# Kernel optimization log

Measured on AMD Instinct MI355X. Metric: run time of the kernel, lower is better.

## Reference

```python
import jax, jax.numpy as jnp
import numpy as np

OUT = 7          # roi_align output_size
NUM_ANCHORS = 27 # 3 scales x 3 ratios x 3 angles
MAX_PROPOSALS = 100
RPN_STRIDE = 32


def conv2d(x, w, b, stride=1, pad=1):
    y = jax.lax.conv_general_dilated(
        x, w, (stride, stride), [(pad, pad), (pad, pad)],
        dimension_numbers=('NCHW', 'OIHW', 'NCHW'))
    return y + b[None, :, None, None]


def generate_anchors(H, W, stride):
    # matches CustomOrientedRPN.generate_anchors
    sx = np.arange(0, W * stride, stride, dtype=np.float32)
    sy = np.arange(0, H * stride, stride, dtype=np.float32)
    SY, SX = np.meshgrid(sy, sx, indexing='ij')
    shifts = np.stack([SX, SY], axis=-1).reshape(-1, 2)  # [HW,2]
    base = []
    for scale in (32.0, 64.0, 128.0):
        for ratio in (0.5, 1.0, 2.0):
            w = scale * ratio ** 0.5
            h = scale / ratio ** 0.5
            for angle in (0.0, 45.0, 90.0):
                base.append([w, h, angle])
    base = np.array(base, dtype=np.float32)  # [A,3]
    A = base.shape[0]
    anchors = np.concatenate(
        [np.repeat(shifts[:, None, :], A, axis=1),
         np.broadcast_to(base[None], (shifts.shape[0], A, 3))], axis=-1)
    return jnp.asarray(anchors.reshape(-1, 5))  # [HW*A, 5]


def rotated_roi_align(features, boxes, batch_idx):
    # Vectorized version of the per-box affine_grid + grid_sample loop
    # (align_corners=False semantics for both, zero padding for grid_sample).
    B, C, Hf, Wf = features.shape
    lin = (2.0 * jnp.arange(OUT, dtype=features.dtype) + 1.0) / OUT - 1.0
    ys, xs = jnp.meshgrid(lin, lin, indexing='ij')  # [7,7] base grid

    cx, cy, w, h, ang = (boxes[:, i] for i in range(5))
    ar = -ang * jnp.pi / 180.0
    c, s = jnp.cos(ar), jnp.sin(ar)
    t00 = w / Wf * c; t01 = -h / Hf * s; t02 = 2.0 * cx / Wf - 1.0
    t10 = w / Wf * s; t11 = h / Hf * c;  t12 = 2.0 * cy / Hf - 1.0
    gx = t00[:, None, None] * xs + t01[:, None, None] * ys + t02[:, None, None]  # [N,7,7]
    gy = t10[:, None, None] * xs + t11[:, None, None] * ys + t12[:, None, None]

    ix = ((gx + 1.0) * Wf - 1.0) / 2.0
    iy = ((gy + 1.0) * Hf - 1.0) / 2.0
    x0 = jnp.floor(ix); y0 = jnp.floor(iy)
    wx = ix - x0;       wy = iy - y0
    x0i = x0.astype(jnp.int32); y0i = y0.astype(jnp.int32)

    def gather(dx, dy, wgt):
        xi = x0i + dx; yi = y0i + dy
        valid = (xi >= 0) & (xi < Wf) & (yi >= 0) & (yi < Hf)
        xc = jnp.clip(xi, 0, Wf - 1)
        yc = jnp.clip(yi, 0, Hf - 1)
        def one(bi, yb, xb):
            return features[bi][:, yb, xb]  # [C,7,7]
        vals = jax.vmap(one)(batch_idx, yc, xc)  # [N,C,7,7]
        return vals * (wgt * valid)[:, None, :, :]

    return (gather(0, 0, (1 - wx) * (1 - wy)) + gather(1, 0, wx * (1 - wy)) +
            gather(0, 1, (1 - wx) * wy) + gather(1, 1, wx * wy))


def setup_inputs() -> dict:
    key = jax.random.key(0)
    ks = jax.random.split(key, 20)

    def w(k, shape):
        fan_in = int(np.prod(shape[1:]))
        return jax.random.normal(k, shape, jnp.float32) / np.sqrt(fan_in)

    C = 256; A = NUM_ANCHORS; NC = 5
    return {
        'images': jax.random.normal(ks[0], (8, 3, 1024, 1024), jnp.float32),
        'backbone_w': w(ks[1], (C, 3, 3, 3)),   'backbone_b': jnp.zeros((C,), jnp.float32),
        'rpn_conv_w': w(ks[2], (256, C, 3, 3)), 'rpn_conv_b': jnp.zeros((256,), jnp.float32),
        'obj_w': w(ks[3], (A, 256, 1, 1)),      'obj_b': jnp.zeros((A,), jnp.float32),
        'delta_w': w(ks[4], (A * 5, 256, 1, 1)) * 0.1, 'delta_b': jnp.zeros((A * 5,), jnp.float32),
        'fc1_w': w(ks[5], (1024, C * OUT * OUT)), 'fc1_b': jnp.zeros((1024,), jnp.float32),
        'fc2_w': w(ks[6], (1024, 1024)),          'fc2_b': jnp.zeros((1024,), jnp.float32),
        'cls_w': w(ks[7], (NC, 1024)),            'cls_b': jnp.zeros((NC,), jnp.float32),
        'bbox_w': w(ks[8], (5, 1024)),            'bbox_b': jnp.zeros((5,), jnp.float32),
    }


def reference(images, backbone_w, backbone_b, rpn_conv_w, rpn_conv_b,
              obj_w, obj_b, delta_w, delta_b,
              fc1_w, fc1_b, fc2_w, fc2_b, cls_w, cls_b, bbox_w, bbox_b):
    # backbone (stand-in: single stride-16 conv)
    f = conv2d(images, backbone_w, backbone_b, stride=16, pad=1)  # [B,256,64,64]
    B, C, H, W = f.shape
    # F.interpolate(scale_factor=0.5, bilinear, align_corners=False) == 2x2 mean
    f = f.reshape(B, C, H // 2, 2, W // 2, 2).mean(axis=(3, 5))   # [B,256,32,32]
    Hf, Wf = f.shape[2], f.shape[3]

    # RPN
    t = jax.nn.relu(conv2d(f, rpn_conv_w, rpn_conv_b, 1, 1))
    _logits = conv2d(t, obj_w, obj_b, 1, 0)  # computed as in original (unused downstream)
    deltas = conv2d(t, delta_w, delta_b, 1, 0)  # [B, A*5, Hf, Wf]
    A = NUM_ANCHORS
    deltas = deltas.reshape(B, A, 5, Hf, Wf).transpose(0, 3, 4, 1, 2).reshape(B, -1, 5)

    anchors = generate_anchors(Hf, Wf, RPN_STRIDE)  # [HW*A,5]
    acx, acy, aw, ah, aa = (anchors[:, i] for i in range(5))
    pcx = deltas[:, :, 0] * aw + acx
    pcy = deltas[:, :, 1] * ah + acy
    pw = jnp.exp(deltas[:, :, 2]) * aw
    ph = jnp.exp(deltas[:, :, 3]) * ah
    pa = aa + deltas[:, :, 4]
    proposals = jnp.stack([pcx, pcy, pw, ph, pa], axis=-1)  # [B, HW*A, 5]
    proposals = proposals[:, :MAX_PROPOSALS]                # p[:max_proposals]

    boxes = proposals.reshape(-1, 5)                        # [B*100, 5]
    batch_idx = jnp.repeat(jnp.arange(B), MAX_PROPOSALS)
    pooled = rotated_roi_align(f, boxes, batch_idx)         # [B*100, 256, 7, 7]

    x = pooled.reshape(pooled.shape[0], -1)
    x = jax.nn.relu(x @ fc1_w.T + fc1_b)
    x = jax.nn.relu(x @ fc2_w.T + fc2_b)
    class_logits = x @ cls_w.T + cls_b
    obb_preds = x @ bbox_w.T + bbox_b
    return class_logits, obb_preds
```

## Files before the change

### kernel.cpp

```cpp
#include <hip/hip_runtime.h>
#include <hip/hip_bf16.h>

using bf16 = __hip_bfloat16;

typedef __attribute__((ext_vector_type(8))) short bf16x8;
typedef __attribute__((ext_vector_type(4))) float f32x4;

__device__ __forceinline__ void async16(const void* g, void* l) {
  __builtin_amdgcn_global_load_lds(
      (const __attribute__((address_space(1))) unsigned int*)g,
      (__attribute__((address_space(3))) unsigned int*)l, 16, 0, 0);
}

__device__ __forceinline__ void store_o(float* C, size_t i, float v) { C[i] = v; }
__device__ __forceinline__ void store_o(bf16* C, size_t i, float v) {
  C[i] = __float2bfloat16(v);
}

__global__ __launch_bounds__(256) void k_backbone(const float* __restrict__ img,
    const float* __restrict__ w, const float* __restrict__ bias,
    float* __restrict__ f) {
  int blk = blockIdx.x;
  int x = blk & 31, y = (blk >> 5) & 31, b = blk >> 10;
  __shared__ float patch[4 * 27];
  int t = threadIdx.x;
  if (t < 108) {
    int kx = t % 3, ky = (t / 3) % 3, cin = (t / 9) % 3, sub = t / 27;
    int sy = sub >> 1, sx = sub & 1;
    int iy = (2 * y + sy) * 16 - 1 + ky;
    int ix = (2 * x + sx) * 16 - 1 + kx;
    float v = 0.f;
    if (iy >= 0 && ix >= 0)
      v = img[((size_t)(b * 3 + cin) * 1024 + iy) * 1024 + ix];
    patch[t] = v;
  }
  __syncthreads();
  int c = t;
  float wr[27];
#pragma unroll
  for (int k = 0; k < 27; ++k) wr[k] = w[c * 27 + k];
  float acc = 0.f;
#pragma unroll
  for (int sub = 0; sub < 4; ++sub)
#pragma unroll
    for (int k = 0; k < 27; ++k)
      acc += patch[sub * 27 + k] * wr[k];
  f[(size_t)blk * 256 + c] = acc * 0.25f + bias[c];
}

__global__ __launch_bounds__(256) void k_rpn(const float* __restrict__ f,
    const float* __restrict__ rpn_w, float* __restrict__ part) {
  int p = blockIdx.x;
  int kc = blockIdx.y;
  int x = p & 3, b = p >> 2;
  __shared__ float fpl[6][16];
  int tid = threadIdx.x;
  if (tid < 96) {
    int cin2 = tid & 15;
    int rc = tid >> 4;
    int row = rc / 3, col = rc % 3;
    int xc = x - 1 + col;
    float v = 0.f;
    if (xc >= 0)
      v = f[((size_t)(b * 32 + row) * 32 + xc) * 256 + kc * 16 + cin2];
    fpl[rc][cin2] = v;
  }
  __syncthreads();
  int c = tid;
  const float* wbase = rpn_w + (size_t)c * 2304 + kc * 144;
  float acc = 0.f;
#pragma unroll
  for (int cin2 = 0; cin2 < 16; ++cin2) {
    const float* wp = wbase + cin2 * 9;
    acc += fpl[0][cin2] * wp[3] + fpl[1][cin2] * wp[4]
         + fpl[2][cin2] * wp[5] + fpl[3][cin2] * wp[6]
         + fpl[4][cin2] * wp[7] + fpl[5][cin2] * wp[8];
  }
  part[((size_t)kc * 32 + p) * 256 + c] = acc;
}

__global__ __launch_bounds__(512) void k_delta(const float* __restrict__ part,
    const float* __restrict__ rpn_b,
    const float* __restrict__ dw, const float* __restrict__ db,
    float* __restrict__ boxes) {
  int p = blockIdx.x;
  int x = p & 3, b = p >> 2;
  __shared__ float tbuf[256];
  __shared__ float dvals[135];
  int tid = threadIdx.x;
  if (tid < 256) {
    float s = rpn_b[tid];
#pragma unroll
    for (int kc = 0; kc < 16; ++kc)
      s += part[((size_t)kc * 32 + p) * 256 + tid];
    tbuf[tid] = fmaxf(s, 0.f);
  }
  __syncthreads();
  if (tid < 270) {
    int o = tid >> 1, half = tid & 1;
    const float* wp = dw + (size_t)o * 256 + half * 128;
    const float* tp = tbuf + half * 128;
    float s = 0.f;
#pragma unroll 8
    for (int k = 0; k < 128; ++k) s += tp[k] * wp[k];
    s += __shfl_xor(s, 1, 64);
    if (half == 0) dvals[o] = s + db[o];
  }
  __syncthreads();
  if (tid < 27) {
    int i = x * 27 + tid;
    if (i < 100) {
      int a = tid;
      int si = a / 9, ri = (a / 3) % 3, ai = a % 3;
      float scale = 32.f * (float)(1 << si);
      float sr = (ri == 0) ? 0.70710678118654752f : (ri == 1 ? 1.0f : 1.41421356237309505f);
      float aw = scale * sr, ah = scale / sr;
      float aang = 45.f * (float)ai;
      float acx = 32.f * (float)x, acy = 0.f;
      float* bx = boxes + (size_t)(b * 100 + i) * 5;
      bx[0] = dvals[a * 5 + 0] * aw + acx;
      bx[1] = dvals[a * 5 + 1] * ah + acy;
      bx[2] = expf(dvals[a * 5 + 2]) * aw;
      bx[3] = expf(dvals[a * 5 + 3]) * ah;
      bx[4] = aang + dvals[a * 5 + 4];
    }
  }
}

__global__ __launch_bounds__(256) void k_roialign(const float* __restrict__ f,
    const float* __restrict__ boxes, bf16* __restrict__ pooled) {
  int n = blockIdx.x;
  int b = n / 100;
  __shared__ int six[49], siy[49];
  __shared__ float swx[49], swy[49];
  __shared__ float pool_s[12544];
  int tid = threadIdx.x;
  if (tid < 49) {
    float cx = boxes[n * 5 + 0], cy = boxes[n * 5 + 1];
    float w = boxes[n * 5 + 2], h = boxes[n * 5 + 3], ang = boxes[n * 5 + 4];
    float ar = -ang * 0.017453292519943295f;
    float cc = cosf(ar), ss = sinf(ar);
    float t00 = w * (1.f / 32.f) * cc, t01 = -h * (1.f / 32.f) * ss;
    float t02 = cx * (2.f / 32.f) - 1.f;
    float t10 = w * (1.f / 32.f) * ss, t11 = h * (1.f / 32.f) * cc;
    float t12 = cy * (2.f / 32.f) - 1.f;
    int py = tid / 7, px = tid - py * 7;
    float lx = (2.f * px + 1.f) * (1.f / 7.f) - 1.f;
    float ly = (2.f * py + 1.f) * (1.f / 7.f) - 1.f;
    float gx = t00 * lx + t01 * ly + t02;
    float gy = t10 * lx + t11 * ly + t12;
    float ix = ((gx + 1.f) * 32.f - 1.f) * 0.5f;
    float iy = ((gy + 1.f) * 32.f - 1.f) * 0.5f;
    float x0 = floorf(ix), y0 = floorf(iy);
    six[tid] = (int)x0; siy[tid] = (int)y0;
    swx[tid] = ix - x0; swy[tid] = iy - y0;
  }
  __syncthreads();
  const float* fb = f + (size_t)b * 262144;
  int c = tid;
  for (int bin = 0; bin < 49; ++bin) {
    int x0 = six[bin], y0 = siy[bin];
    float wx = swx[bin], wy = swy[bin];
    float acc = 0.f;
    if (x0 >= 0 && x0 < 32 && y0 >= 0 && y0 < 32)
      acc += fb[(y0 * 32 + x0) * 256 + c] * ((1.f - wx) * (1.f - wy));
    if (x0 + 1 >= 0 && x0 + 1 < 32 && y0 >= 0 && y0 < 32)
      acc += fb[(y0 * 32 + x0 + 1) * 256 + c] * (wx * (1.f - wy));
    if (x0 >= 0 && x0 < 32 && y0 + 1 >= 0 && y0 + 1 < 32)
      acc += fb[((y0 + 1) * 32 + x0) * 256 + c] * ((1.f - wx) * wy);
    if (x0 + 1 >= 0 && x0 + 1 < 32 && y0 + 1 >= 0 && y0 + 1 < 32)
      acc += fb[((y0 + 1) * 32 + x0 + 1) * 256 + c] * (wx * wy);
    pool_s[c * 49 + bin] = acc;
  }
  __syncthreads();
  bf16* po = pooled + (size_t)n * 12544;
  for (int k = tid; k < 12544; k += 256) po[k] = __float2bfloat16(pool_s[k]);
}

__global__ __launch_bounds__(256) void k_gemm_sk(
    const unsigned short* __restrict__ A, const float* __restrict__ B,
    float* __restrict__ P, int M, int N, int K, int KC) {
  __shared__ unsigned short As[64 * 64];
  __shared__ unsigned short Bs[64 * 72];
  int t = threadIdx.x;
  int wv = t >> 6, ln = t & 63;
  int quad = ln >> 4, l15 = ln & 15;
  int n0 = blockIdx.x * 64, m0 = blockIdx.y * 64;
  int kbeg = blockIdx.z * KC;
  int kend = kbeg + KC; if (kend > K) kend = K;

  int arow = wv * 8 + (ln >> 3);
  int sg = (ln & 7) ^ (arow & 7);
  int r0 = m0 + arow;      if (r0 > M - 1) r0 = M - 1;
  int r1 = m0 + arow + 32; if (r1 > M - 1) r1 = M - 1;
  const unsigned short* Ap0 = A + (size_t)r0 * K + sg * 8;
  const unsigned short* Ap1 = A + (size_t)r1 * K + sg * 8;
  unsigned short* ldsA0 = &As[wv * 512];
  unsigned short* ldsA1 = &As[2048 + wv * 512];

  int brow = t >> 2, bq = t & 3;
  const float* Bp = B + (size_t)(n0 + brow) * K + bq * 16;
  unsigned short* bdst = &Bs[brow * 72 + bq * 16];

  f32x4 acc[4];
#pragma unroll
  for (int j = 0; j < 4; ++j) acc[j] = (f32x4){0.f, 0.f, 0.f, 0.f};

  int mrow = wv * 16 + l15;

  for (int k0 = kbeg; k0 < kend; k0 += 64) {
    float4 bv0 = *(const float4*)(Bp + k0);
    float4 bv1 = *(const float4*)(Bp + k0 + 4);
    float4 bv2 = *(const float4*)(Bp + k0 + 8);
    float4 bv3 = *(const float4*)(Bp + k0 + 12);
    __syncthreads();
    async16(Ap0 + k0, ldsA0);
    async16(Ap1 + k0, ldsA1);
    unsigned short bb[16];
    bb[0]  = __bfloat16_as_ushort(__float2bfloat16(bv0.x));
    bb[1]  = __bfloat16_as_ushort(__float2bfloat16(bv0.y));
    bb[2]  = __bfloat16_as_ushort(__float2bfloat16(bv0.z));
    bb[3]  = __bfloat16_as_ushort(__float2bfloat16(bv0.w));
    bb[4]  = __bfloat16_as_ushort(__float2bfloat16(bv1.x));
    bb[5]  = __bfloat16_as_ushort(__float2bfloat16(bv1.y));
    bb[6]  = __bfloat16_as_ushort(__float2bfloat16(bv1.z));
    bb[7]  = __bfloat16_as_ushort(__float2bfloat16(bv1.w));
    bb[8]  = __bfloat16_as_ushort(__float2bfloat16(bv2.x));
    bb[9]  = __bfloat16_as_ushort(__float2bfloat16(bv2.y));
    bb[10] = __bfloat16_as_ushort(__float2bfloat16(bv2.z));
    bb[11] = __bfloat16_as_ushort(__float2bfloat16(bv2.w));
    bb[12] = __bfloat16_as_ushort(__float2bfloat16(bv3.x));
    bb[13] = __bfloat16_as_ushort(__float2bfloat16(bv3.y));
    bb[14] = __bfloat16_as_ushort(__float2bfloat16(bv3.z));
    bb[15] = __bfloat16_as_ushort(__float2bfloat16(bv3.w));
#pragma unroll
    for (int u = 0; u < 2; ++u)
      *(bf16x8*)(bdst + u * 8) = *(const bf16x8*)(bb + u * 8);
    __syncthreads();
#pragma unroll
    for (int ks = 0; ks < 2; ++ks) {
      bf16x8 a = *(const bf16x8*)&As[mrow * 64 + (((ks * 4 + quad) ^ (mrow & 7)) * 8)];
#pragma unroll
      for (int j = 0; j < 4; ++j) {
        bf16x8 b = *(const bf16x8*)&Bs[(j * 16 + l15) * 72 + ks * 32 + quad * 8];
        acc[j] = __builtin_amdgcn_mfma_f32_16x16x32_bf16(a, b, acc[j], 0, 0, 0);
      }
    }
  }
  float* Pz = P + (size_t)blockIdx.z * M * N;
#pragma unroll
  for (int j = 0; j < 4; ++j) {
    int n = n0 + j * 16 + l15;
#pragma unroll
    for (int r = 0; r < 4; ++r) {
      int m = m0 + wv * 16 + quad * 4 + r;
      if (m < M) Pz[(size_t)m * N + n] = acc[j][r];
    }
  }
}

template <typename OutT, int KS>
__global__ __launch_bounds__(256) void k_reduce(const float* __restrict__ P,
    const float* __restrict__ bias, OutT* __restrict__ C, int MN, int N) {
  int i = blockIdx.x * 256 + threadIdx.x;
  if (i * 4 >= MN) return;
  f32x4 s = *(const f32x4*)(P + (size_t)i * 4);
#pragma unroll
  for (int z = 1; z < KS; ++z)
    s += *(const f32x4*)(P + (size_t)z * MN + i * 4);
  int n = (i * 4) % N;
#pragma unroll
  for (int u = 0; u < 4; ++u)
    store_o(C, (size_t)i * 4 + u, fmaxf(s[u] + bias[n + u], 0.f));
}

__global__ __launch_bounds__(640) void k_heads(const float* __restrict__ x2,
    const float* __restrict__ cls_w, const float* __restrict__ cls_b,
    const float* __restrict__ bbox_w, const float* __restrict__ bbox_b,
    float* __restrict__ out) {
  int n = blockIdx.x;
  int wave = threadIdx.x >> 6;
  int lane = threadIdx.x & 63;
  const float* w = (wave < 5) ? (cls_w + (size_t)wave * 1024)
                              : (bbox_w + (size_t)(wave - 5) * 1024);
  const float* xr = x2 + (size_t)n * 1024;
  float s = 0.f;
  for (int k = lane; k < 1024; k += 64) s += xr[k] * w[k];
  for (int off = 32; off; off >>= 1) s += __shfl_down(s, off, 64);
  if (lane == 0) {
    int o = (wave < 5) ? wave : wave - 5;
    float bias = (wave < 5) ? cls_b[o] : bbox_b[o];
    int base = (wave < 5) ? 0 : 4000;
    out[base + n * 5 + o] = s + bias;
  }
}

extern "C" void kernel_launch(void* const* d_in, const int* in_sizes, int n_in,
                              void* d_out, int out_size, void* d_ws, size_t ws_size,
                              hipStream_t stream) {
  const float* images     = (const float*)d_in[0];
  const float* backbone_w = (const float*)d_in[1];
  const float* backbone_b = (const float*)d_in[2];
  const float* rpn_w      = (const float*)d_in[3];
  const float* rpn_b      = (const float*)d_in[4];
  const float* delta_w    = (const float*)d_in[7];
  const float* delta_b    = (const float*)d_in[8];
  const float* fc1_w      = (const float*)d_in[9];
  const float* fc1_b      = (const float*)d_in[10];
  const float* fc2_w      = (const float*)d_in[11];
  const float* fc2_b      = (const float*)d_in[12];
  const float* cls_w      = (const float*)d_in[13];
  const float* cls_b      = (const float*)d_in[14];
  const float* bbox_w     = (const float*)d_in[15];
  const float* bbox_b     = (const float*)d_in[16];

  char* ws = (char*)d_ws;
  float* f      = (float*)ws;
  float* boxes  = (float*)(ws + 8388608);
  bf16*  pooled = (bf16*) (ws + 8404992);
  bf16*  x1     = (bf16*) (ws + 28475392);
  float* x2     = (float*)(ws + 30113792);
  float* parts  = (float*)(ws + 33390592);
  float* rpart = parts;

  k_backbone<<<8192, 256, 0, stream>>>(images, backbone_w, backbone_b, f);
  k_rpn<<<dim3(32, 16), 256, 0, stream>>>(f, rpn_w, rpart);
  k_delta<<<32, 512, 0, stream>>>(rpart, rpn_b, delta_w, delta_b, boxes);
  k_roialign<<<800, 256, 0, stream>>>(f, boxes, pooled);

  k_gemm_sk<<<dim3(16, 13, 6), 256, 0, stream>>>(
      (const unsigned short*)pooled, fc1_w, parts, 800, 1024, 12544, 2112);
  k_reduce<bf16, 6><<<800, 256, 0, stream>>>(parts, fc1_b, x1, 819200, 1024);

  k_gemm_sk<<<dim3(16, 13, 4), 256, 0, stream>>>(
      (const unsigned short*)x1, fc2_w, parts, 800, 1024, 1024, 256);
  k_reduce<float, 4><<<800, 256, 0, stream>>>(parts, fc2_b, x2, 819200, 1024);

  k_heads<<<800, 640, 0, stream>>>(x2, cls_w, cls_b, bbox_w, bbox_b, (float*)d_out);
}
```

Measured before the change: 353.9 us.

## Enlarge split-K GEMM M-tile to 128 with 2x2 warp layout

The split-K GEMM block tile grows from 64x64 to 128x64, and the four waves are arranged 2x2 so each computes a 64x32 sub-tile with 4x2 MFMA fragments. Each fp32 B (weight) tile, which is loaded and converted to bf16 per block, is now reused across twice as many rows. That halves the number of blocks along M (13 to 7) and the redundant weight reads and conversions. The cost is more accumulator registers, more LDS, fewer blocks in the grid, and more padded rows (896 vs 800).

```diff
diff --git a/kernel.cpp b/kernel.cpp
--- a/kernel.cpp
+++ b/kernel.cpp
@@ -180,33 +180,35 @@
 __global__ __launch_bounds__(256) void k_gemm_sk(
     const unsigned short* __restrict__ A, const float* __restrict__ B,
     float* __restrict__ P, int M, int N, int K, int KC) {
-  __shared__ unsigned short As[64 * 64];
+  __shared__ unsigned short As[128 * 64];
   __shared__ unsigned short Bs[64 * 72];
   int t = threadIdx.x;
   int wv = t >> 6, ln = t & 63;
   int quad = ln >> 4, l15 = ln & 15;
-  int n0 = blockIdx.x * 64, m0 = blockIdx.y * 64;
+  int wm = wv >> 1, wn = wv & 1;
+  int n0 = blockIdx.x * 64, m0 = blockIdx.y * 128;
   int kbeg = blockIdx.z * KC;
   int kend = kbeg + KC; if (kend > K) kend = K;
 
-  int arow = wv * 8 + (ln >> 3);
-  int sg = (ln & 7) ^ (arow & 7);
-  int r0 = m0 + arow;      if (r0 > M - 1) r0 = M - 1;
-  int r1 = m0 + arow + 32; if (r1 > M - 1) r1 = M - 1;
-  const unsigned short* Ap0 = A + (size_t)r0 * K + sg * 8;
-  const unsigned short* Ap1 = A + (size_t)r1 * K + sg * 8;
-  unsigned short* ldsA0 = &As[wv * 512];
-  unsigned short* ldsA1 = &As[2048 + wv * 512];
+  int srow = ln >> 3;
+  int sg = (ln & 7) ^ srow;
+  const unsigned short* Ap[4];
+#pragma unroll
+  for (int q = 0; q < 4; ++q) {
+    int r = m0 + q * 32 + wv * 8 + srow;
+    if (r > M - 1) r = M - 1;
+    Ap[q] = A + (size_t)r * K + sg * 8;
+  }
 
   int brow = t >> 2, bq = t & 3;
   const float* Bp = B + (size_t)(n0 + brow) * K + bq * 16;
   unsigned short* bdst = &Bs[brow * 72 + bq * 16];
 
-  f32x4 acc[4];
-#pragma unroll
-  for (int j = 0; j < 4; ++j) acc[j] = (f32x4){0.f, 0.f, 0.f, 0.f};
-
-  int mrow = wv * 16 + l15;
+  f32x4 acc[4][2];
+#pragma unroll
+  for (int mf = 0; mf < 4; ++mf)
+#pragma unroll
+    for (int nf = 0; nf < 2; ++nf) acc[mf][nf] = (f32x4){0.f, 0.f, 0.f, 0.f};
 
   for (int k0 = kbeg; k0 < kend; k0 += 64) {
     float4 bv0 = *(const float4*)(Bp + k0);
@@ -214,8 +216,9 @@
     float4 bv2 = *(const float4*)(Bp + k0 + 8);
     float4 bv3 = *(const float4*)(Bp + k0 + 12);
     __syncthreads();
-    async16(Ap0 + k0, ldsA0);
-    async16(Ap1 + k0, ldsA1);
+#pragma unroll
+    for (int q = 0; q < 4; ++q)
+      async16(Ap[q] + k0, &As[q * 2048 + wv * 512]);
     unsigned short bb[16];
     bb[0]  = __bfloat16_as_ushort(__float2bfloat16(bv0.x));
     bb[1]  = __bfloat16_as_ushort(__float2bfloat16(bv0.y));
@@ -239,22 +242,32 @@
     __syncthreads();
 #pragma unroll
     for (int ks = 0; ks < 2; ++ks) {
-      bf16x8 a = *(const bf16x8*)&As[mrow * 64 + (((ks * 4 + quad) ^ (mrow & 7)) * 8)];
-#pragma unroll
-      for (int j = 0; j < 4; ++j) {
-        bf16x8 b = *(const bf16x8*)&Bs[(j * 16 + l15) * 72 + ks * 32 + quad * 8];
-        acc[j] = __builtin_amdgcn_mfma_f32_16x16x32_bf16(a, b, acc[j], 0, 0, 0);
+      bf16x8 a[4];
+#pragma unroll
+      for (int mf = 0; mf < 4; ++mf) {
+        int row = wm * 64 + mf * 16 + l15;
+        a[mf] = *(const bf16x8*)&As[row * 64 + (((ks * 4 + quad) ^ (l15 & 7)) * 8)];
+      }
+#pragma unroll
+      for (int nf = 0; nf < 2; ++nf) {
+        bf16x8 b = *(const bf16x8*)&Bs[(wn * 32 + nf * 16 + l15) * 72 + ks * 32 + quad * 8];
+#pragma unroll
+        for (int mf = 0; mf < 4; ++mf)
+          acc[mf][nf] = __builtin_amdgcn_mfma_f32_16x16x32_bf16(a[mf], b, acc[mf][nf], 0, 0, 0);
       }
     }
   }
   float* Pz = P + (size_t)blockIdx.z * M * N;
 #pragma unroll
-  for (int j = 0; j < 4; ++j) {
-    int n = n0 + j * 16 + l15;
-#pragma unroll
-    for (int r = 0; r < 4; ++r) {
-      int m = m0 + wv * 16 + quad * 4 + r;
-      if (m < M) Pz[(size_t)m * N + n] = acc[j][r];
+  for (int nf = 0; nf < 2; ++nf) {
+    int n = n0 + wn * 32 + nf * 16 + l15;
+#pragma unroll
+    for (int mf = 0; mf < 4; ++mf) {
+#pragma unroll
+      for (int r = 0; r < 4; ++r) {
+        int m = m0 + wm * 64 + mf * 16 + quad * 4 + r;
+        if (m < M) Pz[(size_t)m * N + n] = acc[mf][nf][r];
+      }
     }
   }
 }
@@ -328,11 +341,11 @@
   k_delta<<<32, 512, 0, stream>>>(rpart, rpn_b, delta_w, delta_b, boxes);
   k_roialign<<<800, 256, 0, stream>>>(f, boxes, pooled);
 
-  k_gemm_sk<<<dim3(16, 13, 6), 256, 0, stream>>>(
+  k_gemm_sk<<<dim3(16, 7, 6), 256, 0, stream>>>(
       (const unsigned short*)pooled, fc1_w, parts, 800, 1024, 12544, 2112);
   k_reduce<bf16, 6><<<800, 256, 0, stream>>>(parts, fc1_b, x1, 819200, 1024);
 
-  k_gemm_sk<<<dim3(16, 13, 4), 256, 0, stream>>>(
+  k_gemm_sk<<<dim3(16, 7, 4), 256, 0, stream>>>(
       (const unsigned short*)x1, fc2_w, parts, 800, 1024, 1024, 256);
   k_reduce<float, 4><<<800, 256, 0, stream>>>(parts, fc2_b, x2, 819200, 1024);
 
```

New measurement: 336.4 us. 5.0% less time.
